# Optimization experiments

Measured on AMD Instinct MI355X. Metric: run time of the kernel, lower is better.

## Reference

```python
import jax, jax.numpy as jnp
import numpy as np

S, I = 64, 128

def _images():
    # 27 periodic image offsets in [-1,0,1]^3, same ordering as the torch module
    r = jnp.arange(-1.0, 2.0)
    a, b, c = jnp.meshgrid(r, r, r, indexing='ij')
    return jnp.stack([a.ravel(), b.ravel(), c.ravel()], axis=-1)  # [27,3]


def setup_inputs() -> dict:
    key = jax.random.key(0)
    k1, k2, k3 = jax.random.split(key, 3)
    fcoords1 = jax.random.uniform(k1, (S, I, 3), dtype=jnp.float32)
    fcoords2 = jax.random.uniform(k2, (S, I, 3), dtype=jnp.float32)
    matrix = jax.random.normal(k3, (S, 3, 3), dtype=jnp.float32)
    return {"fcoords1": fcoords1, "fcoords2": fcoords2, "matrix": matrix}


def reference(fcoords1, fcoords2, matrix):
    eps = jnp.asarray(1e-10, fcoords1.dtype)
    imgs = _images().astype(matrix.dtype)                      # [27,3]
    cart_coords = jnp.einsum('sij,sjk->sik', fcoords1 % 1, matrix)  # [S,I,3]
    cart1 = cart_coords
    cart2 = jnp.einsum('sij,sjk->sik', fcoords2 % 1, matrix)        # [S,I,3]
    cart_im = jnp.einsum('ij,sjk->sik', imgs, matrix)               # [S,27,3]
    # diff[s,i,j,m,:] = cart2[s,i] - cart1[s,j] + cart_im[s,m]
    d = (cart2[:, :, None, None, :] - cart1[:, None, :, None, :]
         + cart_im[:, None, None, :, :])                            # [S,I,I,27,3]
    dm = jnp.min(jnp.sum(d * d, axis=-1), axis=-1)                  # [S,I,I]
    return jnp.sqrt(dm + eps), cart_coords
```

## Files before the change

kernel.cpp:

```cpp
#include <hip/hip_runtime.h>
#include <math.h>

constexpr int S_ = 64;
constexpr int I_ = 128;
constexpr int PAIRS = I_ * I_;
constexpr int TILES = 8;
constexpr int PAIRS_PER_TILE = PAIRS / TILES;
constexpr int THREADS = 256;
constexpr int PAIRS_PER_THREAD = PAIRS_PER_TILE / THREADS;

__global__ __launch_bounds__(THREADS) void diffdist_kernel(
    const float* __restrict__ f1,
    const float* __restrict__ f2,
    const float* __restrict__ M,
    float* __restrict__ out)
{
    const int s    = blockIdx.x >> 3;
    const int tile = blockIdx.x & (TILES - 1);
    const int tid  = threadIdx.x;

    __shared__ float sm[9];
    __shared__ float c1[I_][3];
    __shared__ float c2[I_][3];

    if (tid < 9) sm[tid] = M[s * 9 + tid];
    __syncthreads();

    {
        const int row = tid & (I_ - 1);
        const float* fsrc = (tid < I_) ? f1 : f2;
        const float* p = fsrc + (size_t)(s * I_ + row) * 3;
        float a = p[0]; a -= floorf(a);
        float b = p[1]; b -= floorf(b);
        float g = p[2]; g -= floorf(g);
        float x = a * sm[0] + b * sm[3] + g * sm[6];
        float y = a * sm[1] + b * sm[4] + g * sm[7];
        float z = a * sm[2] + b * sm[5] + g * sm[8];
        if (tid < I_) {
            c1[row][0] = x; c1[row][1] = y; c1[row][2] = z;
            if (tile == 0) {
                float* o2 = out + (size_t)S_ * PAIRS + (size_t)(s * I_ + row) * 3;
                o2[0] = x; o2[1] = y; o2[2] = z;
            }
        } else {
            c2[row][0] = x; c2[row][1] = y; c2[row][2] = z;
        }
    }
    __syncthreads();

    const float m00 = sm[0], m01 = sm[1], m02 = sm[2];
    const float m10 = sm[3], m11 = sm[4], m12 = sm[5];
    const float m20 = sm[6], m21 = sm[7], m22 = sm[8];

    float* od = out + (size_t)s * PAIRS;

    #pragma unroll
    for (int p = 0; p < PAIRS_PER_THREAD; ++p) {
        const int gidx = tile * PAIRS_PER_TILE + p * THREADS + tid;
        const int i = gidx >> 7;
        const int j = gidx & (I_ - 1);

        const float bx = c2[i][0] - c1[j][0];
        const float by = c2[i][1] - c1[j][1];
        const float bz = c2[i][2] - c1[j][2];

        float best = 3.4e38f;
        #pragma unroll
        for (int ia = -1; ia <= 1; ++ia) {
            const float fa = (float)ia;
            const float ax = fmaf(fa, m00, bx);
            const float ay = fmaf(fa, m01, by);
            const float az = fmaf(fa, m02, bz);
            #pragma unroll
            for (int ib = -1; ib <= 1; ++ib) {
                const float fb = (float)ib;
                const float ux = fmaf(fb, m10, ax);
                const float uy = fmaf(fb, m11, ay);
                const float uz = fmaf(fb, m12, az);
                #pragma unroll
                for (int ic = -1; ic <= 1; ++ic) {
                    const float fc = (float)ic;
                    const float vx = fmaf(fc, m20, ux);
                    const float vy = fmaf(fc, m21, uy);
                    const float vz = fmaf(fc, m22, uz);
                    const float d = fmaf(vx, vx, fmaf(vy, vy, vz * vz));
                    best = fminf(best, d);
                }
            }
        }
        od[gidx] = sqrtf(best + 1e-10f);
    }
}

extern "C" void kernel_launch(void* const* d_in, const int* in_sizes, int n_in,
                              void* d_out, int out_size, void* d_ws, size_t ws_size,
                              hipStream_t stream) {
    const float* f1 = (const float*)d_in[0];
    const float* f2 = (const float*)d_in[1];
    const float* M  = (const float*)d_in[2];
    float* out = (float*)d_out;

    dim3 grid(S_ * TILES);
    dim3 block(THREADS);
    diffdist_kernel<<<grid, block, 0, stream>>>(f1, f2, M, out);
}
```

Measured before the change: 12.09 us.

## Expand image distances algebraically and exploit ± image symmetry

Rewrites |b+t|^2 as |b|^2 + |t|^2 + 2 b·t and pairs each image with its negation, so only 13 precomputed image terms are used per pair instead of 27 full distance evaluations. The image terms are made wave-uniform via readfirstlane. The matrix is read directly into registers rather than staged through shared memory with an extra barrier, and each thread caches its c1 row once. The expansion can lose precision to cancellation for near-zero distances, which the code handles by clamping at zero.

New measurement: 10.69 us. -11.6%, faster.

```diff
diff --git a/kernel.cpp b/kernel.cpp
--- a/kernel.cpp
+++ b/kernel.cpp
@@ -7,7 +7,11 @@
 constexpr int TILES = 8;
 constexpr int PAIRS_PER_TILE = PAIRS / TILES;
 constexpr int THREADS = 256;
-constexpr int PAIRS_PER_THREAD = PAIRS_PER_TILE / THREADS;
+constexpr int PPT = PAIRS_PER_TILE / THREADS;
+
+__device__ __forceinline__ float rfl(float x) {
+    return __int_as_float(__builtin_amdgcn_readfirstlane(__float_as_int(x)));
+}
 
 __global__ __launch_bounds__(THREADS) void diffdist_kernel(
     const float* __restrict__ f1,
@@ -19,12 +23,13 @@
     const int tile = blockIdx.x & (TILES - 1);
     const int tid  = threadIdx.x;
 
-    __shared__ float sm[9];
     __shared__ float c1[I_][3];
     __shared__ float c2[I_][3];
 
-    if (tid < 9) sm[tid] = M[s * 9 + tid];
-    __syncthreads();
+    const float* Ms = M + s * 9;
+    const float m00 = Ms[0], m01 = Ms[1], m02 = Ms[2];
+    const float m10 = Ms[3], m11 = Ms[4], m12 = Ms[5];
+    const float m20 = Ms[6], m21 = Ms[7], m22 = Ms[8];
 
     {
         const int row = tid & (I_ - 1);
@@ -33,9 +38,9 @@
         float a = p[0]; a -= floorf(a);
         float b = p[1]; b -= floorf(b);
         float g = p[2]; g -= floorf(g);
-        float x = a * sm[0] + b * sm[3] + g * sm[6];
-        float y = a * sm[1] + b * sm[4] + g * sm[7];
-        float z = a * sm[2] + b * sm[5] + g * sm[8];
+        float x = fmaf(a, m00, fmaf(b, m10, g * m20));
+        float y = fmaf(a, m01, fmaf(b, m11, g * m21));
+        float z = fmaf(a, m02, fmaf(b, m12, g * m22));
         if (tid < I_) {
             c1[row][0] = x; c1[row][1] = y; c1[row][2] = z;
             if (tile == 0) {
@@ -46,49 +51,49 @@
             c2[row][0] = x; c2[row][1] = y; c2[row][2] = z;
         }
     }
+
+    constexpr int IA[13] = {0, 0, 0, 0,  1,  1, 1,  1, 1, 1,  1, 1, 1};
+    constexpr int IB[13] = {0, 1, 1, 1, -1, -1,-1,  0, 0, 0,  1, 1, 1};
+    constexpr int IC[13] = {1,-1, 0, 1, -1,  0, 1, -1, 0, 1, -1, 0, 1};
+
+    float t2x[13], t2y[13], t2z[13], cc[13];
+    #pragma unroll
+    for (int m = 0; m < 13; ++m) {
+        const float fa = (float)IA[m], fb = (float)IB[m], fc = (float)IC[m];
+        const float tx = fa * m00 + fb * m10 + fc * m20;
+        const float ty = fa * m01 + fb * m11 + fc * m21;
+        const float tz = fa * m02 + fb * m12 + fc * m22;
+        cc[m]  = rfl(fmaf(tx, tx, fmaf(ty, ty, tz * tz)));
+        t2x[m] = rfl(tx + tx);
+        t2y[m] = rfl(ty + ty);
+        t2z[m] = rfl(tz + tz);
+    }
+
     __syncthreads();
 
-    const float m00 = sm[0], m01 = sm[1], m02 = sm[2];
-    const float m10 = sm[3], m11 = sm[4], m12 = sm[5];
-    const float m20 = sm[6], m21 = sm[7], m22 = sm[8];
+    const int j  = tid & (I_ - 1);
+    const int hi = tid >> 7;
+    const float c1x = c1[j][0], c1y = c1[j][1], c1z = c1[j][2];
 
-    float* od = out + (size_t)s * PAIRS;
+    float* od = out + (size_t)s * PAIRS + tile * PAIRS_PER_TILE;
 
     #pragma unroll
-    for (int p = 0; p < PAIRS_PER_THREAD; ++p) {
-        const int gidx = tile * PAIRS_PER_TILE + p * THREADS + tid;
-        const int i = gidx >> 7;
-        const int j = gidx & (I_ - 1);
+    for (int p = 0; p < PPT; ++p) {
+        const int ii = tile * 16 + p * 2 + hi;
+        const float bx = c2[ii][0] - c1x;
+        const float by = c2[ii][1] - c1y;
+        const float bz = c2[ii][2] - c1z;
+        const float n  = fmaf(bx, bx, fmaf(by, by, bz * bz));
 
-        const float bx = c2[i][0] - c1[j][0];
-        const float by = c2[i][1] - c1[j][1];
-        const float bz = c2[i][2] - c1[j][2];
-
-        float best = 3.4e38f;
+        float best = 0.0f;
         #pragma unroll
-        for (int ia = -1; ia <= 1; ++ia) {
-            const float fa = (float)ia;
-            const float ax = fmaf(fa, m00, bx);
-            const float ay = fmaf(fa, m01, by);
-            const float az = fmaf(fa, m02, bz);
-            #pragma unroll
-            for (int ib = -1; ib <= 1; ++ib) {
-                const float fb = (float)ib;
-                const float ux = fmaf(fb, m10, ax);
-                const float uy = fmaf(fb, m11, ay);
-                const float uz = fmaf(fb, m12, az);
-                #pragma unroll
-                for (int ic = -1; ic <= 1; ++ic) {
-                    const float fc = (float)ic;
-                    const float vx = fmaf(fc, m20, ux);
-                    const float vy = fmaf(fc, m21, uy);
-                    const float vz = fmaf(fc, m22, uz);
-                    const float d = fmaf(vx, vx, fmaf(vy, vy, vz * vz));
-                    best = fminf(best, d);
-                }
-            }
+        for (int m = 0; m < 13; ++m) {
+            const float u  = fmaf(bx, t2x[m], fmaf(by, t2y[m], bz * t2z[m]));
+            const float d1 = cc[m] + u;
+            const float d2 = cc[m] - u;
+            best = fminf(best, fminf(d1, d2));
         }
-        od[gidx] = sqrtf(best + 1e-10f);
+        od[p * THREADS + tid] = sqrtf(fmaxf(n + best, 0.0f) + 1e-10f);
     }
 }
 
```
